# Optimization experiments

Hardware: AMD Instinct MI355X
Metric: run time of the kernel (lower is better)

Reference implementation:

```python
import jax, jax.numpy as jnp
import numpy as np

EMBED = 1024
HEADS = 16
HEAD_DIM = EMBED // HEADS

def setup_inputs() -> dict:
    key = jax.random.key(0)
    ks = jax.random.split(key, 9)
    N, Q, K = 2, 2048, 2048
    queries = jax.random.normal(ks[0], (N, Q, EMBED), dtype=jnp.float32)
    keys_ = jax.random.normal(ks[1], (N, K, EMBED), dtype=jnp.float32)
    values = jax.random.normal(ks[2], (N, K, EMBED), dtype=jnp.float32)
    mask = jax.random.randint(ks[3], (N, 1, Q, K), 0, 2, dtype=jnp.int32)
    s = 1.0 / np.sqrt(EMBED)
    Wq = jax.random.normal(ks[4], (EMBED, EMBED), dtype=jnp.float32) * s
    Wk = jax.random.normal(ks[5], (EMBED, EMBED), dtype=jnp.float32) * s
    Wv = jax.random.normal(ks[6], (EMBED, EMBED), dtype=jnp.float32) * s
    Wo = jax.random.normal(ks[7], (EMBED, EMBED), dtype=jnp.float32) * s
    bo = jax.random.normal(ks[8], (EMBED,), dtype=jnp.float32) * s
    return {"queries": queries, "keys": keys_, "values": values, "mask": mask,
            "Wq": Wq, "Wk": Wk, "Wv": Wv, "Wo": Wo, "bo": bo}

def reference(queries, keys, values, mask, Wq, Wk, Wv, Wo, bo):
    N, Qlen, _ = queries.shape
    Klen = keys.shape[1]
    # Linear projections (torch Linear: x @ W.T), then split heads
    q = (queries @ Wq.T).reshape(N, Qlen, HEADS, HEAD_DIM)
    k = (keys @ Wk.T).reshape(N, Klen, HEADS, HEAD_DIM)
    v = (values @ Wv.T).reshape(N, Klen, HEADS, HEAD_DIM)
    energy = jnp.einsum('nqhd,nkhd->nhqk', q, k)  # [N,H,Q,K]
    energy = jnp.where(mask == 0, jnp.float32(-1e20), energy)
    # NOTE: original scales by sqrt(embed_size), not sqrt(head_dim)
    attention = jax.nn.softmax(energy / jnp.sqrt(jnp.float32(EMBED)), axis=3)
    out = jnp.einsum('nhqk,nkhd->nqhd', attention, v).reshape(N, Qlen, EMBED)
    return out @ Wo.T + bo
```

## Files before the change

### kernel.cpp

```cpp
#include <hip/hip_runtime.h>
#include <stdint.h>
#include <stddef.h>

typedef __attribute__((ext_vector_type(8)))  short bf16x8;
typedef __attribute__((ext_vector_type(2)))  float f32x2;
typedef __attribute__((ext_vector_type(4)))  float f32x4;
typedef __attribute__((ext_vector_type(16))) float f32x16;
typedef __attribute__((ext_vector_type(4)))  float float4v;
typedef __attribute__((ext_vector_type(4)))  int   int4v;

#define DEV static __device__ __forceinline__

static constexpr int EMBED  = 1024;
static constexpr int HEADS  = 16;
static constexpr int SEQ    = 2048;

DEV short f2bf(float f) {
  union { float f; unsigned u; } x; x.f = f;
  unsigned r = x.u + 0x7fffu + ((x.u >> 16) & 1u);
  return (short)(r >> 16);
}

DEV int cvtpk(float a, float b) {
  int r; asm("v_cvt_pk_bf16_f32 %0, %1, %2" : "=v"(r) : "v"(a), "v"(b)); return r;
}

DEV float fexp2(float x) { float r; asm("v_exp_f32 %0, %1" : "=v"(r) : "v"(x)); return r; }

#define MFMA16(a,b,c) __builtin_amdgcn_mfma_f32_16x16x32_bf16((a),(b),(c),0,0,0)
#define MFMA32(a,b,c) __builtin_amdgcn_mfma_f32_32x32x16_bf16((a),(b),(c),0,0,0)
#define GLDS(g,l) __builtin_amdgcn_global_load_lds( \
    (const __attribute__((address_space(1))) void*)(g), \
    (__attribute__((address_space(3))) void*)(l), 16, 0, 0)
#define SBAR0() __builtin_amdgcn_sched_barrier(0)
#define ZERO16 {0,0,0,0,0,0,0,0,0,0,0,0,0,0,0,0}
#define ROT3(x) ((x) == 2 ? 0 : (x) + 1)


struct CvtArgs { const float* src[7]; short* dst[7]; int n[7]; };

__global__ void cvt_bf16(CvtArgs a) {
  const int task = blockIdx.y;
  const int i = (blockIdx.x * 256 + threadIdx.x) * 8;
  if (i >= a.n[task]) return;
  const float4v* s = (const float4v*)(a.src[task] + i);
  float4v x = s[0], y = s[1];
  bf16x8 o;
  o[0] = f2bf(x[0]); o[1] = f2bf(x[1]); o[2] = f2bf(x[2]); o[3] = f2bf(x[3]);
  o[4] = f2bf(y[0]); o[5] = f2bf(y[1]); o[6] = f2bf(y[2]); o[7] = f2bf(y[3]);
  *(bf16x8*)(a.dst[task] + i) = o;
}

__global__ void maskpack(const int* __restrict__ m, unsigned long long* __restrict__ out) {
  const int gw = (blockIdx.x * 256 + threadIdx.x) >> 6;
  const int l  = threadIdx.x & 63;
  const int n = gw >> 16, kvblk = (gw >> 11) & 31, q = gw & 2047;
  int v = m[((size_t)n * SEQ + q) * SEQ + kvblk * 64 + l];
  unsigned long long b = __ballot(v != 0);
  if (l == 0) out[((size_t)n * 32 + kvblk) * SEQ + q] = b;
}

template<int MODE>
DEV void gemm_core(const int vv, const short* __restrict__ A, const short* __restrict__ B,
                   short* __restrict__ Cb, float* __restrict__ Cf,
                   const float* __restrict__ bias, short* As, short* Bs)
{
  const int t = threadIdx.x;
  const int l = t & 63, w = t >> 6;
  const int lr = l & 15, lh = l >> 4;
  const int m0 = (vv >> 3) * 128, n0 = (vv & 7) * 128;
  const int wr = w >> 1, wc = w & 1;
  f32x4 acc[4][4] = {};

  const int rA = t >> 2, cA = (t & 3) * 8;
  const short* gA  = A + (size_t)(m0 + rA) * 1024 + cA;
  const short* gA2 = gA + (size_t)64 * 1024;
  const short* gB  = B + (size_t)(n0 + rA) * 1024 + cA;
  const short* gB2 = gB + (size_t)64 * 1024;

  GLDS(gA,       As + w * 512);
  GLDS(gA2,      As + 2048 + w * 512);
  GLDS(gB,       Bs + w * 512);
  GLDS(gB2,      Bs + 2048 + w * 512);
  SBAR0();
  GLDS(gA + 32,  As + 4096 + w * 512);
  GLDS(gA2 + 32, As + 4096 + 2048 + w * 512);
  GLDS(gB + 32,  Bs + 4096 + w * 512);
  GLDS(gB2 + 32, Bs + 4096 + 2048 + w * 512);
  SBAR0();

  int cb = 0, sb = 2;
  #pragma unroll 1
  for (int it = 0; it < 32; ++it) {
    if (it < 31) { asm volatile("s_waitcnt vmcnt(4)" ::: "memory"); }
    else         { asm volatile("s_waitcnt vmcnt(0)" ::: "memory"); }
    SBAR0();
    __builtin_amdgcn_s_barrier();
    SBAR0();
    if (it < 30) {
      const int kt = (it + 2) * 32;
      GLDS(gA + kt,  As + sb * 4096 + w * 512);
      GLDS(gA2 + kt, As + sb * 4096 + 2048 + w * 512);
      GLDS(gB + kt,  Bs + sb * 4096 + w * 512);
      GLDS(gB2 + kt, Bs + sb * 4096 + 2048 + w * 512);
      SBAR0();
    }

    const short* as = As + cb * 4096;
    const short* bs = Bs + cb * 4096;
    bf16x8 af[4], bq[4];
    #pragma unroll
    for (int i = 0; i < 4; ++i)
      af[i] = *(const bf16x8*)&as[(wr * 64 + i * 16 + lr) * 32 + lh * 8];
    #pragma unroll
    for (int i = 0; i < 4; ++i)
      bq[i] = *(const bf16x8*)&bs[(wc * 64 + i * 16 + lr) * 32 + lh * 8];
    #pragma unroll
    for (int mi = 0; mi < 4; ++mi)
      #pragma unroll
      for (int ni = 0; ni < 4; ++ni)
        acc[mi][ni] = MFMA16(af[mi], bq[ni], acc[mi][ni]);

    SBAR0();
    cb = ROT3(cb); sb = ROT3(sb);
  }

  #pragma unroll
  for (int mi = 0; mi < 4; ++mi)
    #pragma unroll
    for (int ni = 0; ni < 4; ++ni)
      #pragma unroll
      for (int r = 0; r < 4; ++r) {
        const int m = m0 + wr * 64 + mi * 16 + lh * 4 + r;
        const int e = n0 + wc * 64 + ni * 16 + lr;
        const float v = acc[mi][ni][r];
        const int nb = m >> 11, s = m & 2047, hh = e >> 6, d = e & 63;
        if (MODE == 0) {
          Cb[(((size_t)(nb * HEADS + hh)) * SEQ + s) * 64 + d] = f2bf(v);
        } else if (MODE == 2) {
          Cb[(((size_t)(nb * HEADS + hh)) * SEQ + s) * 64 + (d ^ ((s & 7) << 3))] = f2bf(v);
        } else if (MODE == 3) {
          Cb[(((size_t)(nb * HEADS + hh)) * 32 + (s >> 6)) * 4096 + d * 64 +
             ((s & 63) ^ ((d & 7) << 3))] = f2bf(v);
        } else {
          Cf[(size_t)m * EMBED + e] = v + bias[e];
        }
      }
}

__global__ __launch_bounds__(256, 2)
void gemm_qkv(const short* __restrict__ Ab, const short* __restrict__ Bb,
              short* __restrict__ Qp, short* __restrict__ Kp, short* __restrict__ VTp)
{
  __shared__ short As[3][4096];
  __shared__ short Bs[3][4096];
  const int lin = blockIdx.x;
  const int s = lin >> 8, j = lin & 255;
  const int vv = (j & 7) * 32 + (j >> 3);
  const short* A = Ab + (size_t)s * 4194304;
  const short* B = Bb + (size_t)s * 1048576;
  if (s == 0)      gemm_core<0>(vv, A, B, Qp,  nullptr, nullptr, &As[0][0], &Bs[0][0]);
  else if (s == 1) gemm_core<2>(vv, A, B, Kp,  nullptr, nullptr, &As[0][0], &Bs[0][0]);
  else             gemm_core<3>(vv, A, B, VTp, nullptr, nullptr, &As[0][0], &Bs[0][0]);
}

__global__ __launch_bounds__(256, 2)
void gemm_out(const short* __restrict__ A, const short* __restrict__ B,
              float* __restrict__ Cf, const float* __restrict__ bias)
{
  __shared__ short As[3][4096];
  __shared__ short Bs[3][4096];
  const int lin = blockIdx.x;
  const int vv = (lin & 7) * 32 + (lin >> 3);
  gemm_core<1>(vv, A, B, nullptr, Cf, bias, &As[0][0], &Bs[0][0]);
}

__global__ __launch_bounds__(256, 2)
void attn256(const short* __restrict__ Qp, const short* __restrict__ Kp,
             const short* __restrict__ VTp, const unsigned long long* __restrict__ MbT,
             short* __restrict__ Aout)
{
  __shared__ short lds[3][8192];

  const int t = threadIdx.x, l = t & 63, w = t >> 6;
  const int lq = l & 31, hi = l >> 5;
  const int lin = blockIdx.x;
  const int vv = (lin & 7) * 64 + (lin >> 3);
  const int hl = vv >> 4, qb = vv & 15;
  const int n = hl >> 4, h = hl & 15;
  const int q0 = qb * 128;
  const int myq = q0 + w * 32 + lq;
  const size_t hb = (size_t)(n * HEADS + h) * SEQ * 64;
  const short* Qh = Qp + hb;
  const unsigned long long* Mh = MbT + (size_t)n * (32 * SEQ);
  const float SCL = 0.045084220027780106f;

  bf16x8 qf[4];
  #pragma unroll
  for (int ks = 0; ks < 4; ++ks)
    qf[ks] = *(const bf16x8*)(Qh + (size_t)myq * 64 + ks * 16 + hi * 8);

  const short ONE = (short)0x3F80;
  const bf16x8 onesv = {ONE, ONE, ONE, ONE, ONE, ONE, ONE, ONE};
  const f32x16 zerov = ZERO16;

  f32x16 acco[2] = { ZERO16, ZERO16 };
  f32x16 accl = ZERO16;

  const short* kgp = Kp + hb + w * 1024 + l * 8;
  const short* vgp = VTp + hb + w * 1024 + l * 8;
  const unsigned long long* mp = MbT + (size_t)n * (32 * SEQ) + myq;

  unsigned long long mw = *mp; mp += SEQ;
  SBAR0();
  GLDS(kgp,        &lds[0][w * 1024]);
  GLDS(kgp + 512,  &lds[0][w * 1024 + 512]);
  GLDS(vgp,        &lds[0][4096 + w * 1024]);
  GLDS(vgp + 512,  &lds[0][4096 + w * 1024 + 512]);
  SBAR0();
  GLDS(kgp + 4096, &lds[1][w * 1024]);
  GLDS(kgp + 4608, &lds[1][w * 1024 + 512]);
  GLDS(vgp + 4096, &lds[1][4096 + w * 1024]);
  GLDS(vgp + 4608, &lds[1][4096 + w * 1024 + 512]);
  SBAR0();
  kgp += 8192; vgp += 8192;

  int cb = 0, sb = 2;
  #pragma unroll 1
  for (int tt = 0; tt < 32; ++tt) {
    if (tt < 31) { asm volatile("s_waitcnt vmcnt(4)" ::: "memory"); }
    else         { asm volatile("s_waitcnt vmcnt(0)" ::: "memory"); }
    SBAR0();
    __builtin_amdgcn_s_barrier();
    SBAR0();

    unsigned long long mw_next = 0;
    if (tt < 31) {
      mw_next = *mp; mp += SEQ;
      SBAR0();
    }
    if (tt < 30) {
      GLDS(kgp,       &lds[sb][w * 1024]);
      GLDS(kgp + 512, &lds[sb][w * 1024 + 512]);
      GLDS(vgp,       &lds[sb][4096 + w * 1024]);
      GLDS(vgp + 512, &lds[sb][4096 + w * 1024 + 512]);
      kgp += 4096; vgp += 4096;
      SBAR0();
    }

    const short* Ks  = &lds[cb][0];
    const short* VTs = &lds[cb][4096];

    #pragma unroll
    for (int half = 0; half < 2; ++half) {
      f32x16 sacc;
      __builtin_amdgcn_s_setprio(1);
      #pragma unroll
      for (int ks = 0; ks < 4; ++ks) {
        const int d = ks * 16 + hi * 8;
        bf16x8 kf = *(const bf16x8*)&Ks[(half * 32 + lq) * 64 + (d ^ ((lq & 7) << 3))];
        sacc = MFMA32(kf, qf[ks], ks == 0 ? zerov : sacc);
      }
      __builtin_amdgcn_s_setprio(0);
      const unsigned mmw = ~(unsigned)(mw >> (half * 32 + hi * 4));
      float p[16];
      #pragma unroll
      for (int r = 0; r < 16; ++r) {
        const int idx = (r & 3) + 8 * (r >> 2);
        union { int i; float f; } b;
        b.i = __builtin_amdgcn_sbfe(mmw, idx, 1) & 0xC3480000;
        p[r] = fexp2(__builtin_fmaf(sacc[r], SCL, b.f));
      }
      bf16x8 pf[2];
      #pragma unroll
      for (int kb = 0; kb < 2; ++kb) {
        int x1 = cvtpk(p[kb * 8 + 0], p[kb * 8 + 1]);
        int y1 = cvtpk(p[kb * 8 + 4], p[kb * 8 + 5]);
        int x2 = cvtpk(p[kb * 8 + 2], p[kb * 8 + 3]);
        int y2 = cvtpk(p[kb * 8 + 6], p[kb * 8 + 7]);
        asm("v_permlane32_swap_b32 %0, %1" : "+v"(x1), "+v"(y1));
        asm("v_permlane32_swap_b32 %0, %1" : "+v"(x2), "+v"(y2));
        union { int w4[4]; bf16x8 v; } u;
        u.w4[0] = x1; u.w4[1] = x2; u.w4[2] = y1; u.w4[3] = y2;
        pf[kb] = u.v;
      }
      __builtin_amdgcn_s_setprio(1);
      accl = MFMA32(onesv, pf[0], accl);
      accl = MFMA32(onesv, pf[1], accl);
      #pragma unroll
      for (int dt = 0; dt < 2; ++dt) {
        const int d = dt * 32 + lq;
        #pragma unroll
        for (int kb = 0; kb < 2; ++kb) {
          const int kv = half * 32 + kb * 16 + hi * 8;
          bf16x8 vf = *(const bf16x8*)&VTs[d * 64 + (kv ^ ((d & 7) << 3))];
          acco[dt] = MFMA32(vf, pf[kb], acco[dt]);
        }
      }
      __builtin_amdgcn_s_setprio(0);
    }
    mw = mw_next;
    SBAR0();
    cb = ROT3(cb); sb = ROT3(sb);
  }

  const float invs = 1.f / (accl[0] + 1e-30f);

  short* ot = &lds[0][0] + w * 2048;
  #pragma unroll
  for (int dt = 0; dt < 2; ++dt)
    #pragma unroll
    for (int r = 0; r < 16; ++r) {
      const int d = dt * 32 + (r & 3) + 8 * (r >> 2) + 4 * hi;
      ot[lq * 64 + (d ^ ((lq & 7) << 3))] = f2bf(acco[dt][r] * invs);
    }
  __syncthreads();

  const int qq = l >> 1, hb2 = l & 1;
  #pragma unroll
  for (int it = 0; it < 4; ++it) {
    const int didx = (hb2 * 32 + it * 8) ^ ((qq & 7) << 3);
    bf16x8 v = *(const bf16x8*)&ot[qq * 64 + didx];
    *(bf16x8*)&Aout[((size_t)(n * SEQ + q0 + w * 32 + qq)) * EMBED + h * 64 + hb2 * 32 + it * 8] = v;
  }
}

extern "C" void kernel_launch(void* const* d_in, const int* in_sizes, int n_in,
                              void* d_out, int out_size, void* d_ws, size_t ws_size,
                              hipStream_t stream) {
  (void)in_sizes; (void)n_in; (void)out_size;
  const float* queries = (const float*)d_in[0];
  const float* keys    = (const float*)d_in[1];
  const float* values  = (const float*)d_in[2];
  const int*   mask    = (const int*)d_in[3];
  const float* Wq      = (const float*)d_in[4];
  const float* Wk      = (const float*)d_in[5];
  const float* Wv      = (const float*)d_in[6];
  const float* Wo      = (const float*)d_in[7];
  const float* bo      = (const float*)d_in[8];

  const size_t NEED = (size_t)76 * 1024 * 1024;
  if (ws_size < NEED) return;

  char* ws = (char*)d_ws;
  short* qb   = (short*)(ws + 0);
  short* kb   = (short*)(ws + (8u << 20));
  short* vb   = (short*)(ws + (16u << 20));
  short* wqb  = (short*)(ws + (24u << 20));
  short* wkb  = (short*)(ws + (26u << 20));
  short* wvb  = (short*)(ws + (28u << 20));
  short* wob  = (short*)(ws + (30u << 20));
  unsigned long long* mbits = (unsigned long long*)(ws + (32u << 20));
  short* Qp   = (short*)(ws + (40u << 20));
  short* Kp   = (short*)(ws + (48u << 20));
  short* VTp  = (short*)(ws + (56u << 20));
  short* ao   = (short*)(ws + (64u << 20));

  const int NTOK = 2 * SEQ * EMBED;
  const int NW   = EMBED * EMBED;

  CvtArgs ca;
  ca.src[0] = queries; ca.dst[0] = qb;  ca.n[0] = NTOK;
  ca.src[1] = keys;    ca.dst[1] = kb;  ca.n[1] = NTOK;
  ca.src[2] = values;  ca.dst[2] = vb;  ca.n[2] = NTOK;
  ca.src[3] = Wq;      ca.dst[3] = wqb; ca.n[3] = NW;
  ca.src[4] = Wk;      ca.dst[4] = wkb; ca.n[4] = NW;
  ca.src[5] = Wv;      ca.dst[5] = wvb; ca.n[5] = NW;
  ca.src[6] = Wo;      ca.dst[6] = wob; ca.n[6] = NW;
  cvt_bf16<<<dim3(2048, 7), 256, 0, stream>>>(ca);

  maskpack<<<dim3(32768), 256, 0, stream>>>(mask, mbits);

  gemm_qkv<<<dim3(768), 256, 0, stream>>>(qb, wqb, Qp, Kp, VTp);

  attn256<<<dim3(512), 256, 0, stream>>>(Qp, Kp, VTp, mbits, ao);

  gemm_out<<<dim3(256), 256, 0, stream>>>(ao, wob, (float*)d_out, bo);
}
```

Measured before the change: 146.5 us.

## Split attention over two KV halves with a separate combine kernel

The attention kernel now splits each (head, query-block) into two halves along the key/value axis. This doubles the grid to 1024 blocks and raises launch bounds to 4 blocks per CU, with LDS cut from triple to double buffering. Each half writes an unnormalized bf16 partial output and its row sum, and a new combine kernel adds the two halves and normalizes. The aim is more resident waves per CU to hide latency. The cost is an extra kernel launch, extra global traffic for the partials, two block barriers per iteration, and some bf16 rounding of the unnormalized partials.

```diff
diff --git a/kernel.cpp b/kernel.cpp
--- a/kernel.cpp
+++ b/kernel.cpp
@@ -19,6 +19,10 @@
   union { float f; unsigned u; } x; x.f = f;
   unsigned r = x.u + 0x7fffu + ((x.u >> 16) & 1u);
   return (short)(r >> 16);
+}
+
+DEV float bf2f(short s) {
+  union { unsigned u; float f; } x; x.u = (unsigned)(unsigned short)s << 16; return x.f;
 }
 
 DEV int cvtpk(float a, float b) {
@@ -175,24 +179,25 @@
   gemm_core<1>(vv, A, B, nullptr, Cf, bias, &As[0][0], &Bs[0][0]);
 }
 
-__global__ __launch_bounds__(256, 2)
-void attn256(const short* __restrict__ Qp, const short* __restrict__ Kp,
-             const short* __restrict__ VTp, const unsigned long long* __restrict__ MbT,
-             short* __restrict__ Aout)
+__global__ __launch_bounds__(256, 4)
+void attn_part(const short* __restrict__ Qp, const short* __restrict__ Kp,
+               const short* __restrict__ VTp, const unsigned long long* __restrict__ MbT,
+               short* __restrict__ Op, float* __restrict__ Ls)
 {
-  __shared__ short lds[3][8192];
+  __shared__ short lds[2][8192];
 
   const int t = threadIdx.x, l = t & 63, w = t >> 6;
   const int lq = l & 31, hi = l >> 5;
   const int lin = blockIdx.x;
-  const int vv = (lin & 7) * 64 + (lin >> 3);
-  const int hl = vv >> 4, qb = vv & 15;
+  const int vv = (lin & 7) * 128 + (lin >> 3);
+  const int hl = vv >> 5;
+  const int kvhalf = (vv >> 4) & 1;
+  const int qb = vv & 15;
   const int n = hl >> 4, h = hl & 15;
   const int q0 = qb * 128;
   const int myq = q0 + w * 32 + lq;
   const size_t hb = (size_t)(n * HEADS + h) * SEQ * 64;
   const short* Qh = Qp + hb;
-  const unsigned long long* Mh = MbT + (size_t)n * (32 * SEQ);
   const float SCL = 0.045084220027780106f;
 
   bf16x8 qf[4];
@@ -207,49 +212,42 @@
   f32x16 acco[2] = { ZERO16, ZERO16 };
   f32x16 accl = ZERO16;
 
-  const short* kgp = Kp + hb + w * 1024 + l * 8;
-  const short* vgp = VTp + hb + w * 1024 + l * 8;
-  const unsigned long long* mp = MbT + (size_t)n * (32 * SEQ) + myq;
+  const short* kgp = Kp + hb + (size_t)kvhalf * 65536 + w * 1024 + l * 8;
+  const short* vgp = VTp + hb + (size_t)kvhalf * 65536 + w * 1024 + l * 8;
+  const unsigned long long* mp = MbT + (size_t)n * (32 * SEQ) + (size_t)(kvhalf * 16) * SEQ + myq;
 
   unsigned long long mw = *mp; mp += SEQ;
-  SBAR0();
-  GLDS(kgp,        &lds[0][w * 1024]);
-  GLDS(kgp + 512,  &lds[0][w * 1024 + 512]);
-  GLDS(vgp,        &lds[0][4096 + w * 1024]);
-  GLDS(vgp + 512,  &lds[0][4096 + w * 1024 + 512]);
-  SBAR0();
-  GLDS(kgp + 4096, &lds[1][w * 1024]);
-  GLDS(kgp + 4608, &lds[1][w * 1024 + 512]);
-  GLDS(vgp + 4096, &lds[1][4096 + w * 1024]);
-  GLDS(vgp + 4608, &lds[1][4096 + w * 1024 + 512]);
-  SBAR0();
-  kgp += 8192; vgp += 8192;
-
-  int cb = 0, sb = 2;
+  {
+    GLDS(kgp,       &lds[0][w * 1024]);
+    GLDS(kgp + 512, &lds[0][w * 1024 + 512]);
+    GLDS(vgp,       &lds[0][4096 + w * 1024]);
+    GLDS(vgp + 512, &lds[0][4096 + w * 1024 + 512]);
+    kgp += 4096; vgp += 4096;
+  }
+
   #pragma unroll 1
-  for (int tt = 0; tt < 32; ++tt) {
-    if (tt < 31) { asm volatile("s_waitcnt vmcnt(4)" ::: "memory"); }
-    else         { asm volatile("s_waitcnt vmcnt(0)" ::: "memory"); }
-    SBAR0();
-    __builtin_amdgcn_s_barrier();
-    SBAR0();
-
+  for (int tt = 0; tt < 16; ++tt) {
     unsigned long long mw_next = 0;
-    if (tt < 31) {
+    if (tt < 15) {
       mw_next = *mp; mp += SEQ;
       SBAR0();
-    }
-    if (tt < 30) {
-      GLDS(kgp,       &lds[sb][w * 1024]);
-      GLDS(kgp + 512, &lds[sb][w * 1024 + 512]);
-      GLDS(vgp,       &lds[sb][4096 + w * 1024]);
-      GLDS(vgp + 512, &lds[sb][4096 + w * 1024 + 512]);
+      const int nb = (tt + 1) & 1;
+      GLDS(kgp,       &lds[nb][w * 1024]);
+      GLDS(kgp + 512, &lds[nb][w * 1024 + 512]);
+      GLDS(vgp,       &lds[nb][4096 + w * 1024]);
+      GLDS(vgp + 512, &lds[nb][4096 + w * 1024 + 512]);
       kgp += 4096; vgp += 4096;
+      asm volatile("s_waitcnt vmcnt(5)" ::: "memory");
+      SBAR0();
+    } else {
+      asm volatile("s_waitcnt vmcnt(0)" ::: "memory");
       SBAR0();
     }
-
-    const short* Ks  = &lds[cb][0];
-    const short* VTs = &lds[cb][4096];
+    __builtin_amdgcn_s_barrier();
+    SBAR0();
+
+    const short* Ks  = &lds[tt & 1][0];
+    const short* VTs = &lds[tt & 1][4096];
 
     #pragma unroll
     for (int half = 0; half < 2; ++half) {
@@ -301,10 +299,9 @@
     }
     mw = mw_next;
     SBAR0();
-    cb = ROT3(cb); sb = ROT3(sb);
+    __builtin_amdgcn_s_barrier();
+    SBAR0();
   }
-
-  const float invs = 1.f / (accl[0] + 1e-30f);
 
   short* ot = &lds[0][0] + w * 2048;
   #pragma unroll
@@ -312,17 +309,37 @@
     #pragma unroll
     for (int r = 0; r < 16; ++r) {
       const int d = dt * 32 + (r & 3) + 8 * (r >> 2) + 4 * hi;
-      ot[lq * 64 + (d ^ ((lq & 7) << 3))] = f2bf(acco[dt][r] * invs);
+      ot[lq * 64 + (d ^ ((lq & 7) << 3))] = f2bf(acco[dt][r]);
     }
+  if (hi == 0) Ls[(size_t)(hl * 2 + kvhalf) * SEQ + myq] = accl[0];
   __syncthreads();
 
   const int qq = l >> 1, hb2 = l & 1;
+  const size_t obase = ((size_t)(hl * 2 + kvhalf) * SEQ + q0 + w * 32 + qq) * 64;
   #pragma unroll
   for (int it = 0; it < 4; ++it) {
     const int didx = (hb2 * 32 + it * 8) ^ ((qq & 7) << 3);
     bf16x8 v = *(const bf16x8*)&ot[qq * 64 + didx];
-    *(bf16x8*)&Aout[((size_t)(n * SEQ + q0 + w * 32 + qq)) * EMBED + h * 64 + hb2 * 32 + it * 8] = v;
+    *(bf16x8*)&Op[obase + hb2 * 32 + it * 8] = v;
   }
+}
+
+__global__ void combine(const short* __restrict__ Op, const float* __restrict__ Ls,
+                        short* __restrict__ ao)
+{
+  const int idx = blockIdx.x * 256 + threadIdx.x;
+  const int dc = idx & 7, q = (idx >> 3) & 2047, hl = idx >> 14;
+  const int n = hl >> 4, h = hl & 15;
+  const float l0 = Ls[(size_t)(hl * 2 + 0) * SEQ + q];
+  const float l1 = Ls[(size_t)(hl * 2 + 1) * SEQ + q];
+  const float inv = 1.f / (l0 + l1 + 1e-30f);
+  const bf16x8 a = *(const bf16x8*)&Op[((size_t)(hl * 2 + 0) * SEQ + q) * 64 + dc * 8];
+  const bf16x8 b = *(const bf16x8*)&Op[((size_t)(hl * 2 + 1) * SEQ + q) * 64 + dc * 8];
+  bf16x8 o;
+  #pragma unroll
+  for (int j = 0; j < 8; ++j)
+    o[j] = f2bf((bf2f(a[j]) + bf2f(b[j])) * inv);
+  *(bf16x8*)&ao[((size_t)(n * SEQ + q)) * EMBED + h * 64 + dc * 8] = o;
 }
 
 extern "C" void kernel_launch(void* const* d_in, const int* in_sizes, int n_in,
@@ -351,10 +368,12 @@
   short* wvb  = (short*)(ws + (28u << 20));
   short* wob  = (short*)(ws + (30u << 20));
   unsigned long long* mbits = (unsigned long long*)(ws + (32u << 20));
+  float* lsum = (float*)(ws + (33u << 20));
   short* Qp   = (short*)(ws + (40u << 20));
   short* Kp   = (short*)(ws + (48u << 20));
   short* VTp  = (short*)(ws + (56u << 20));
   short* ao   = (short*)(ws + (64u << 20));
+  short* Opart = (short*)(ws + 0);
 
   const int NTOK = 2 * SEQ * EMBED;
   const int NW   = EMBED * EMBED;
@@ -373,7 +392,9 @@
 
   gemm_qkv<<<dim3(768), 256, 0, stream>>>(qb, wqb, Qp, Kp, VTp);
 
-  attn256<<<dim3(512), 256, 0, stream>>>(Qp, Kp, VTp, mbits, ao);
+  attn_part<<<dim3(1024), 256, 0, stream>>>(Qp, Kp, VTp, mbits, Opart, lsum);
+
+  combine<<<dim3(2048), 256, 0, stream>>>(Opart, lsum, ao);
 
   gemm_out<<<dim3(256), 256, 0, stream>>>(ao, wob, (float*)d_out, bo);
 }
```

Result: no change. 148.2 us (+1.2%).

## Switch attention K/V staging from triple to double buffering, raise QKV occupancy

Applied to the files above, without the earlier changes.

The attention kernel now stages K/V tiles in two LDS buffers instead of three. Each iteration issues the next tile's load, waits for the current one, and adds a second barrier at the end of the loop so the buffer is not overwritten while still being read. This shrinks LDS per block, which may allow more resident blocks. The trade-off is a shallower prefetch distance and an extra barrier per iteration. Separately, the QKV GEMM launch bounds ask for three blocks per CU instead of two, which may constrain registers.

```diff
diff --git a/kernel.cpp b/kernel.cpp
--- a/kernel.cpp
+++ b/kernel.cpp
@@ -148,7 +148,7 @@
       }
 }
 
-__global__ __launch_bounds__(256, 2)
+__global__ __launch_bounds__(256, 3)
 void gemm_qkv(const short* __restrict__ Ab, const short* __restrict__ Bb,
               short* __restrict__ Qp, short* __restrict__ Kp, short* __restrict__ VTp)
 {
@@ -180,7 +180,7 @@
              const short* __restrict__ VTp, const unsigned long long* __restrict__ MbT,
              short* __restrict__ Aout)
 {
-  __shared__ short lds[3][8192];
+  __shared__ short lds[2][8192];
 
   const int t = threadIdx.x, l = t & 63, w = t >> 6;
   const int lq = l & 31, hi = l >> 5;
@@ -192,7 +192,6 @@
   const int myq = q0 + w * 32 + lq;
   const size_t hb = (size_t)(n * HEADS + h) * SEQ * 64;
   const short* Qh = Qp + hb;
-  const unsigned long long* Mh = MbT + (size_t)n * (32 * SEQ);
   const float SCL = 0.045084220027780106f;
 
   bf16x8 qf[4];
@@ -212,44 +211,37 @@
   const unsigned long long* mp = MbT + (size_t)n * (32 * SEQ) + myq;
 
   unsigned long long mw = *mp; mp += SEQ;
-  SBAR0();
-  GLDS(kgp,        &lds[0][w * 1024]);
-  GLDS(kgp + 512,  &lds[0][w * 1024 + 512]);
-  GLDS(vgp,        &lds[0][4096 + w * 1024]);
-  GLDS(vgp + 512,  &lds[0][4096 + w * 1024 + 512]);
-  SBAR0();
-  GLDS(kgp + 4096, &lds[1][w * 1024]);
-  GLDS(kgp + 4608, &lds[1][w * 1024 + 512]);
-  GLDS(vgp + 4096, &lds[1][4096 + w * 1024]);
-  GLDS(vgp + 4608, &lds[1][4096 + w * 1024 + 512]);
-  SBAR0();
-  kgp += 8192; vgp += 8192;
-
-  int cb = 0, sb = 2;
+  {
+    GLDS(kgp,       &lds[0][w * 1024]);
+    GLDS(kgp + 512, &lds[0][w * 1024 + 512]);
+    GLDS(vgp,       &lds[0][4096 + w * 1024]);
+    GLDS(vgp + 512, &lds[0][4096 + w * 1024 + 512]);
+    kgp += 4096; vgp += 4096;
+  }
+
   #pragma unroll 1
   for (int tt = 0; tt < 32; ++tt) {
-    if (tt < 31) { asm volatile("s_waitcnt vmcnt(4)" ::: "memory"); }
-    else         { asm volatile("s_waitcnt vmcnt(0)" ::: "memory"); }
-    SBAR0();
-    __builtin_amdgcn_s_barrier();
-    SBAR0();
-
     unsigned long long mw_next = 0;
     if (tt < 31) {
       mw_next = *mp; mp += SEQ;
       SBAR0();
-    }
-    if (tt < 30) {
-      GLDS(kgp,       &lds[sb][w * 1024]);
-      GLDS(kgp + 512, &lds[sb][w * 1024 + 512]);
-      GLDS(vgp,       &lds[sb][4096 + w * 1024]);
-      GLDS(vgp + 512, &lds[sb][4096 + w * 1024 + 512]);
+      const int nb = (tt + 1) & 1;
+      GLDS(kgp,       &lds[nb][w * 1024]);
+      GLDS(kgp + 512, &lds[nb][w * 1024 + 512]);
+      GLDS(vgp,       &lds[nb][4096 + w * 1024]);
+      GLDS(vgp + 512, &lds[nb][4096 + w * 1024 + 512]);
       kgp += 4096; vgp += 4096;
+      asm volatile("s_waitcnt vmcnt(5)" ::: "memory");
+      SBAR0();
+    } else {
+      asm volatile("s_waitcnt vmcnt(0)" ::: "memory");
       SBAR0();
     }
-
-    const short* Ks  = &lds[cb][0];
-    const short* VTs = &lds[cb][4096];
+    __builtin_amdgcn_s_barrier();
+    SBAR0();
+
+    const short* Ks  = &lds[tt & 1][0];
+    const short* VTs = &lds[tt & 1][4096];
 
     #pragma unroll
     for (int half = 0; half < 2; ++half) {
@@ -301,7 +293,8 @@
     }
     mw = mw_next;
     SBAR0();
-    cb = ROT3(cb); sb = ROT3(sb);
+    __builtin_amdgcn_s_barrier();
+    SBAR0();
   }
 
   const float invs = 1.f / (accl[0] + 1e-30f);
```

After: 145.6 us. About the same (-0.6%).
